# Optimization experiments

Hardware: AMD Instinct MI355X
Metric: run time of the kernel (lower is better)

## Reference

```python
import jax, jax.numpy as jnp
import numpy as np

N = 50000      # nodes
E = 800000     # edges (before self loops)
F_IN = 50      # PPI num_features
H = 4          # heads
C = 64         # hidden per head
NC = 121       # PPI num_classes
NEG_SLOPE = 0.2


def setup_inputs() -> dict:
    key = jax.random.key(0)
    ks = jax.random.split(key, 20)
    p = lambda k, shape: (jax.random.normal(k, shape, jnp.float32) * 0.1)
    x0 = jax.random.normal(ks[0], (N, F_IN), jnp.float32)
    edge_index = jax.random.randint(ks[1], (2, E), 0, N, dtype=jnp.int64)
    return dict(
        x0=x0, edge_index=edge_index,
        W1=p(ks[2], (F_IN, H * C)), as1=p(ks[3], (H, C)), ad1=p(ks[4], (H, C)),
        res1=p(ks[5], (F_IN, H * C)), b1=jnp.zeros((H * C,), jnp.float32),
        W2=p(ks[6], (H * C, H * C)), as2=p(ks[7], (H, C)), ad2=p(ks[8], (H, C)),
        res2=p(ks[9], (H * C, H * C)), b2=jnp.zeros((H * C,), jnp.float32),
        W3=p(ks[10], (H * C, H * NC)), as3=p(ks[11], (H, NC)), ad3=p(ks[12], (H, NC)),
        res3=p(ks[13], (H * C, NC)), b3=jnp.zeros((NC,), jnp.float32),
    )


def _gat(x, src, dst, W, a_src, a_dst, resW, b, concat):
    """PyG-style GATConv with residual, self loops already in (src, dst)."""
    n = x.shape[0]
    heads, outc = a_src.shape
    h = (x @ W).reshape(n, heads, outc)                 # [N,H,C]
    al_s = (h * a_src).sum(-1)                          # [N,H]
    al_d = (h * a_dst).sum(-1)                          # [N,H]
    e = jax.nn.leaky_relu(al_s[src] + al_d[dst], NEG_SLOPE)  # [E,H]
    m = jax.ops.segment_max(e, dst, num_segments=n)     # stable softmax per dst
    ex = jnp.exp(e - m[dst])
    denom = jax.ops.segment_sum(ex, dst, num_segments=n)
    alpha = ex / denom[dst]                             # [E,H]
    out = jax.ops.segment_sum(h[src] * alpha[:, :, None], dst, num_segments=n)  # [N,H,C]
    out = out.reshape(n, heads * outc) if concat else out.mean(axis=1)
    return out + x @ resW + b


def reference(x0, edge_index,
              W1, as1, ad1, res1, b1,
              W2, as2, ad2, res2, b2,
              W3, as3, ad3, res3, b3):
    n = x0.shape[0]
    loop = jnp.arange(n, dtype=edge_index.dtype)        # add self loops (PyG default)
    src = jnp.concatenate([edge_index[0], loop])
    dst = jnp.concatenate([edge_index[1], loop])
    x1 = jax.nn.relu(_gat(x0, src, dst, W1, as1, ad1, res1, b1, True))
    x2 = jax.nn.relu(_gat(x1, src, dst, W2, as2, ad2, res2, b2, True))
    x3 = _gat(x2, src, dst, W3, as3, ad3, res3, b3, False)
    return x3
```

## Files before the change

### kernel.cpp

```cpp
#include <hip/hip_runtime.h>

#define NNODES 50000
#define NEDGES 800000
#define NTOT   (NEDGES + NNODES)
#define F_IN   50
#define KPAD1  64
#define HEADS  4
#define C1     64
#define HC1    256
#define NC     121
#define K1S    320
#define K3S    1280
#define N2S    512

typedef unsigned short ushort_t;
typedef __attribute__((ext_vector_type(4))) unsigned short ushort4_t;
typedef __attribute__((ext_vector_type(8))) unsigned short ushort8;
typedef __attribute__((ext_vector_type(8))) __bf16 bf16x8;
typedef __attribute__((ext_vector_type(4))) float f32x4;
typedef __attribute__((ext_vector_type(4))) int int4_t;

__device__ __forceinline__ ushort_t f2bf(float f) {
    union { float f; unsigned int u; } v; v.f = f;
    unsigned int u = v.u;
// ... 139 lines not shown
        return;
    }
    i -= SZ_D;
    if (i < SZ_E) {
        int c = i / K3S, kk = i - c * K3S;
        float v;
        if (kk < 1024) {
            int h = kk >> 8, k = kk & 255;
            v = 0.25f * W3[(size_t)k * (HEADS * NC) + h * NC + c];
        } else {
            int k = kk - 1024;
            v = res3[(size_t)k * NC + c];
        }
        Bt3[i] = f2bf(v);
        return;
    }
    i -= SZ_E;
    if (i < 2 * SZ_F) {
        const float* a = (i < SZ_F) ? as1 : ad1;
        float* w = (i < SZ_F) ? w_as1 : w_ad1;
        int ii = (i < SZ_F) ? i : i - SZ_F;
        int k = ii >> 2, h = ii & 3;
        float s = 0.f;
        if (k < F_IN)
            for (int c = 0; c < C1; ++c) s += W1[(size_t)k * HC1 + h * C1 + c] * a[h * C1 + c];
        w[ii] = s;
        return;
    }
    i -= 2 * SZ_F;
    {
        int grp = i / SZ_G, ii = i - grp * SZ_G;
        int k = ii >> 2, h = ii & 3;
        float s = 0.f;
        if (grp < 2) {
            const float* a = grp ? ad2 : as2;
            for (int c = 0; c < C1; ++c) s += W2[(size_t)k * HC1 + h * C1 + c] * a[h * C1 + c];
            (grp ? w_ad2 : w_as2)[ii] = s;
        } else {
            const float* a = (grp == 3) ? ad3 : as3;
            for (int c = 0; c < NC; ++c) s += W3[(size_t)k * (HEADS * NC) + h * NC + c] * a[h * NC + c];
            ((grp == 3) ? w_ad3 : w_as3)[ii] = s;
        }
    }
}

__global__ __launch_bounds__(256)
void prep_count_kernel(const float* __restrict__ x0,
                 const float* __restrict__ W1, const float* __restrict__ res1,
                 const float* __restrict__ W2, const float* __restrict__ res2,
                 const float* __restrict__ W3, const float* __restrict__ res3,
                 const float* __restrict__ as1, const float* __restrict__ ad1,
                 const float* __restrict__ as2, const float* __restrict__ ad2,
                 const float* __restrict__ as3, const float* __restrict__ ad3,
                 const float* __restrict__ b2,
                 ushort_t* __restrict__ x0b, ushort_t* __restrict__ Bt1,
                 ushort_t* __restrict__ Bt2, ushort_t* __restrict__ Bt3,
                 float* __restrict__ bias512,
                 float* __restrict__ w_as1, float* __restrict__ w_ad1,
                 float* __restrict__ w_as2, float* __restrict__ w_ad2,
                 float* __restrict__ w_as3, float* __restrict__ w_ad3,
                 const int* __restrict__ ei, int* __restrict__ cnt) {
    int b = blockIdx.x;
    if (b < PREP_BLK) {
        prep_body(b * 256 + threadIdx.x, x0, W1, res1, W2, res2, W3, res3,
                  as1, ad1, as2, ad2, as3, ad3, b2, x0b, Bt1, Bt2, Bt3,
                  bias512, w_as1, w_ad1, w_as2, w_ad2, w_as3, w_ad3);
    } else {
        count_body((b - PREP_BLK) * 256 + threadIdx.x, ei, cnt);
    }
}

#define BM 128
#define BN 128
#define BK 64
#define LDP (BK + 8)

__global__ __launch_bounds__(256)
void gemm_mfma_kernel(const ushort_t* __restrict__ A1, int lda1,
                      const ushort_t* __restrict__ A2, int lda2, int Ksplit,
                      const ushort_t* __restrict__ Bt, const float* __restrict__ bias,
                      float* __restrict__ Cf, ushort_t* __restrict__ Cb,
                      int M, int N, int K, int relu) {
    __shared__ ushort_t As[BM * LDP];
    __shared__ ushort_t Bs[BN * LDP];
    int tid = threadIdx.x;
    int lane = tid & 63;
    int wid = tid >> 6;
    int wm = (wid & 1) * 64, wn = (wid >> 1) * 64;
    int l15 = lane & 15;
    int q8 = (lane >> 4) * 8;
    int m0 = blockIdx.y * BM, n0 = blockIdx.x * BN;

    f32x4 acc[4][4] = {};

    for (int k0 = 0; k0 < K; k0 += BK) {
        #pragma unroll
        for (int it = 0; it < 4; ++it) {
            int c = tid + it * 256;
            int row = c >> 3, c8 = c & 7;
            int k = k0 + c8 * 8;
            ushort8 va = (ushort8)0;
            int gm = m0 + row;
            if (gm < M) {
                if (k < Ksplit) va = *(const ushort8*)&A1[(size_t)gm * lda1 + k];
                else            va = *(const ushort8*)&A2[(size_t)gm * lda2 + (k - Ksplit)];
            }
            *(ushort8*)&As[row * LDP + c8 * 8] = va;
            ushort8 vb = (ushort8)0;
            int gn = n0 + row;
            if (gn < N) vb = *(const ushort8*)&Bt[(size_t)gn * K + k];
            *(ushort8*)&Bs[row * LDP + c8 * 8] = vb;
        }
        __syncthreads();
        #pragma unroll
        for (int kk = 0; kk < BK; kk += 32) {
            bf16x8 af[4], bfr[4];
            #pragma unroll
            for (int mi = 0; mi < 4; ++mi)
                af[mi] = *(const bf16x8*)&As[(wm + mi * 16 + l15) * LDP + kk + q8];
            #pragma unroll
            for (int ni = 0; ni < 4; ++ni)
                bfr[ni] = *(const bf16x8*)&Bs[(wn + ni * 16 + l15) * LDP + kk + q8];
            #pragma unroll
            for (int mi = 0; mi < 4; ++mi)
                #pragma unroll
                for (int ni = 0; ni < 4; ++ni)
                    acc[mi][ni] = __builtin_amdgcn_mfma_f32_16x16x32_bf16(
                        af[mi], bfr[ni], acc[mi][ni], 0, 0, 0);
        }
        __syncthreads();
    }

    #pragma unroll
    for (int mi = 0; mi < 4; ++mi) {
        int mbase = m0 + wm + mi * 16 + (lane >> 4) * 4;
        #pragma unroll
        for (int ni = 0; ni < 4; ++ni) {
            int ncol = n0 + wn + ni * 16 + l15;
            if (ncol >= N) continue;
            float bv = bias ? bias[ncol] : 0.f;
            #pragma unroll
            for (int r = 0; r < 4; ++r) {
                int m = mbase + r;
                if (m >= M) continue;
                float v = acc[mi][ni][r] + bv;
                if (relu) v = fmaxf(v, 0.f);
                if (Cf) Cf[(size_t)m * N + ncol] = v;
                else    Cb[(size_t)m * N + ncol] = f2bf(v);
            }
        }
    }
}

__device__ __forceinline__ void gemv_body(int n, int lane,
                        const ushort_t* __restrict__ X, int K,
                        const float* __restrict__ w_as, const float* __restrict__ w_ad,
                        float* __restrict__ als, float* __restrict__ ald) {
    float ps[HEADS] = {}, pd[HEADS] = {};
    for (int k0 = lane * 4; k0 < K; k0 += 256) {
        ushort4_t xv = *(const ushort4_t*)&X[(size_t)n * K + k0];
        float x[4] = {bf2f(xv.x), bf2f(xv.y), bf2f(xv.z), bf2f(xv.w)};
        #pragma unroll
        for (int j = 0; j < 4; ++j) {
            #pragma unroll
            for (int h = 0; h < HEADS; ++h) {
                ps[h] += x[j] * w_as[(k0 + j) * 4 + h];
                pd[h] += x[j] * w_ad[(k0 + j) * 4 + h];
            }
        }
    }
    #pragma unroll
    for (int off = 32; off; off >>= 1)
        #pragma unroll
        for (int h = 0; h < HEADS; ++h) {
            ps[h] += __shfl_xor(ps[h], off);
            pd[h] += __shfl_xor(pd[h], off);
        }
    if (lane == 0)
        #pragma unroll
        for (int h = 0; h < HEADS; ++h) {
            als[n * HEADS + h] = ps[h];
            ald[n * HEADS + h] = pd[h];
        }
}

__global__ __launch_bounds__(256)
void logits_gemv_kernel(const ushort_t* __restrict__ X, int K,
                        const float* __restrict__ w_as, const float* __restrict__ w_ad,
                        float* __restrict__ als, float* __restrict__ ald) {
    gemv_body(blockIdx.x * 4 + (threadIdx.x >> 6), threadIdx.x & 63, X, K, w_as, w_ad, als, ald);
}

#define GEMV_BLK (NNODES / 4)
__global__ __launch_bounds__(256)
void scatter_gemv1_kernel(const int* __restrict__ ei, int* __restrict__ cursor,
                          int* __restrict__ csr_src,
                          const ushort_t* __restrict__ X,
                          const float* __restrict__ w_as, const float* __restrict__ w_ad,
                          float* __restrict__ als, float* __restrict__ ald) {
    int b = blockIdx.x;
    if (b < GEMV_BLK) {
        gemv_body(b * 4 + (threadIdx.x >> 6), threadIdx.x & 63, X, KPAD1, w_as, w_ad, als, ald);
    } else {
        scatter_body((b - GEMV_BLK) * 256 + threadIdx.x, ei, cursor, csr_src);
    }
}

#define E_CHUNK_NOMAX(ROWBYTES)                                               \
    int i = base + lane;                                                      \
    int nv = end - base; if (nv > 64) nv = 64;                                \
    if (i < end) {                                                            \
        int s = csr_src[i];                                                   \
        soffw[lane] = s * (ROWBYTES);                                         \
        f32x4 av = *(const f32x4*)&als[s * 4];                                \
        f32x4 e;                                                              \
        _Pragma("unroll")                                                     \
        for (int h = 0; h < HEADS; ++h) {                                     \
            e[h] = __expf(lrelu(av[h] + aldd[h]));                            \
            den4[h] += e[h];                                                  \
        }                                                                     \
        *(f32x4*)&sew[lane * 4] = e;                                          \
    }                                                                         \
    wave_lds_sync();

#define DEN_REDUCE                                                            \
    _Pragma("unroll")                                                         \
    for (int off = 32; off; off >>= 1)                                        \
        _Pragma("unroll")                                                     \
        for (int h = 0; h < HEADS; ++h)                                       \
            den4[h] += __shfl_xor(den4[h], off);

#define AGG_BLOCKS 2048
#define AGG_WAVES  (AGG_BLOCKS * 4)

__global__ __launch_bounds__(256)
void agg1_kernel(const ushort_t* __restrict__ x0b,
                 const float* __restrict__ als, const float* __restrict__ ald,
                 const int* __restrict__ row_ptr, const int* __restrict__ csr_src,
                 ushort_t* __restrict__ aggx) {
    __shared__ int   soff[4][64];
    __shared__ float se[4][64 * 4];
    int wid = threadIdx.x >> 6, lane = threadIdx.x & 63;
    int* soffw = soff[wid];
    float* sew = se[wid];
    int lb = lane * 2;
    for (int d = blockIdx.x * 4 + wid; d < NNODES; d += AGG_WAVES) {
        int beg = row_ptr[d], end = row_ptr[d + 1];
        f32x4 aldd = *(const f32x4*)&ald[d * 4];
        f32x4 den4 = (f32x4)0.f;
        f32x4 acc  = (f32x4)0.f;
        for (int base = beg; base < end; base += 64) {
            E_CHUNK_NOMAX(KPAD1 * 2)
            int j = 0;
            for (; j + 4 <= nv; j += 4) {
                int4_t o = *(const int4_t*)&soffw[j];
                f32x4 e0 = *(const f32x4*)&sew[j * 4];
                f32x4 e1 = *(const f32x4*)&sew[(j + 1) * 4];
                f32x4 e2 = *(const f32x4*)&sew[(j + 2) * 4];
                f32x4 e3 = *(const f32x4*)&sew[(j + 3) * 4];
                float x0v = bf2f(*(const ushort_t*)((const char*)x0b + o.x + lb));
                float x1v = bf2f(*(const ushort_t*)((const char*)x0b + o.y + lb));
                float x2v = bf2f(*(const ushort_t*)((const char*)x0b + o.z + lb));
                float x3v = bf2f(*(const ushort_t*)((const char*)x0b + o.w + lb));
                acc += e0 * x0v + e1 * x1v + e2 * x2v + e3 * x3v;
            }
            for (; j < nv; ++j) {
                int o = soffw[j];
                f32x4 e = *(const f32x4*)&sew[j * 4];
                float xv = bf2f(*(const ushort_t*)((const char*)x0b + o + lb));
                acc += e * xv;
            }
            wave_lds_sync();
        }
        DEN_REDUCE
        #pragma unroll
        for (int h = 0; h < HEADS; ++h)
            aggx[(size_t)d * HC1 + h * 64 + lane] = f2bf(acc[h] / den4[h]);
    }
}

__global__ __launch_bounds__(256)
void agg2_kernel(const ushort_t* __restrict__ comb,
                 const float* __restrict__ als, const float* __restrict__ ald,
                 const int* __restrict__ row_ptr, const int* __restrict__ csr_src,
                 const float* __restrict__ w_as3, const float* __restrict__ w_ad3,
                 ushort_t* __restrict__ xnext,
                 float* __restrict__ als3, float* __restrict__ ald3) {
    __shared__ int   soff[4][64];
    __shared__ float se[4][64 * 4];
    int wid = threadIdx.x >> 6, lane = threadIdx.x & 63;
    int* soffw = soff[wid];
    float* sew = se[wid];
    int hh = lane >> 4;
    int lb = lane * 8;
    for (int d = blockIdx.x * 4 + wid; d < NNODES; d += AGG_WAVES) {
        int beg = row_ptr[d], end = row_ptr[d + 1];
        f32x4 aldd = *(const f32x4*)&ald[d * 4];
        f32x4 den4 = (f32x4)0.f;
        f32x4 acc  = (f32x4)0.f;
        for (int base = beg; base < end; base += 64) {
            E_CHUNK_NOMAX(N2S * 2)
            int j = 0;
            for (; j + 4 <= nv; j += 4) {
                int4_t o = *(const int4_t*)&soffw[j];
                float e0 = sew[j * 4 + hh], e1 = sew[(j + 1) * 4 + hh];
                float e2 = sew[(j + 2) * 4 + hh], e3 = sew[(j + 3) * 4 + hh];
                f32x4 x0v = cvt4(*(const ushort4_t*)((const char*)comb + o.x + lb));
                f32x4 x1v = cvt4(*(const ushort4_t*)((const char*)comb + o.y + lb));
                f32x4 x2v = cvt4(*(const ushort4_t*)((const char*)comb + o.z + lb));
                f32x4 x3v = cvt4(*(const ushort4_t*)((const char*)comb + o.w + lb));
                acc += e0 * x0v + e1 * x1v + e2 * x2v + e3 * x3v;
            }
            for (; j < nv; ++j) {
                int o = soffw[j];
                float e = sew[j * 4 + hh];
                acc += e * cvt4(*(const ushort4_t*)((const char*)comb + o + lb));
            }
            wave_lds_sync();
        }
        DEN_REDUCE
        float r = 1.f / den4[hh];
        ushort4_t rv = *(const ushort4_t*)&comb[(size_t)d * N2S + 256 + lane * 4];
        f32x4 resv = cvt4(rv);
        f32x4 vout;
        #pragma unroll
        for (int c = 0; c < 4; ++c) vout[c] = fmaxf(acc[c] * r + resv[c], 0.f);
        ushort4_t o4;
        o4.x = f2bf(vout[0]); o4.y = f2bf(vout[1]);
        o4.z = f2bf(vout[2]); o4.w = f2bf(vout[3]);
        *(ushort4_t*)&xnext[(size_t)d * HC1 + lane * 4] = o4;
        f32x4 ps = (f32x4)0.f, pd = (f32x4)0.f;
        #pragma unroll
        for (int j = 0; j < 4; ++j) {
            f32x4 wsj = *(const f32x4*)&w_as3[(lane * 4 + j) * 4];
            f32x4 wdj = *(const f32x4*)&w_ad3[(lane * 4 + j) * 4];
            ps += vout[j] * wsj;
            pd += vout[j] * wdj;
        }
        #pragma unroll
        for (int off = 32; off; off >>= 1) {
            #pragma unroll
            for (int h = 0; h < HEADS; ++h) {
                ps[h] += __shfl_xor(ps[h], off);
                pd[h] += __shfl_xor(pd[h], off);
            }
        }
        if (lane == 0) {
            *(f32x4*)&als3[d * 4] = ps;
            *(f32x4*)&ald3[d * 4] = pd;
        }
    }
}

__global__ __launch_bounds__(256)
void agg3_kernel(const ushort_t* __restrict__ x2b,
                 const float* __restrict__ als, const float* __restrict__ ald,
                 const int* __restrict__ row_ptr, const int* __restrict__ csr_src,
                 ushort_t* __restrict__ aggx) {
    __shared__ int   soff[4][64];
    __shared__ float se[4][64 * 4];
    int wid = threadIdx.x >> 6, lane = threadIdx.x & 63;
    int* soffw = soff[wid];
    float* sew = se[wid];
    int lb = lane * 8;
    for (int d = blockIdx.x * 4 + wid; d < NNODES; d += AGG_WAVES) {
        int beg = row_ptr[d], end = row_ptr[d + 1];
        f32x4 aldd = *(const f32x4*)&ald[d * 4];
        f32x4 den4 = (f32x4)0.f;
        f32x4 acc[HEADS] = {};
        for (int base = beg; base < end; base += 64) {
            E_CHUNK_NOMAX(HC1 * 2)
            int j = 0;
            for (; j + 4 <= nv; j += 4) {
                int4_t o = *(const int4_t*)&soffw[j];
                f32x4 e0 = *(const f32x4*)&sew[j * 4];
                f32x4 e1 = *(const f32x4*)&sew[(j + 1) * 4];
                f32x4 e2 = *(const f32x4*)&sew[(j + 2) * 4];
                f32x4 e3 = *(const f32x4*)&sew[(j + 3) * 4];
                f32x4 x0v = cvt4(*(const ushort4_t*)((const char*)x2b + o.x + lb));
                f32x4 x1v = cvt4(*(const ushort4_t*)((const char*)x2b + o.y + lb));
                f32x4 x2v = cvt4(*(const ushort4_t*)((const char*)x2b + o.z + lb));
                f32x4 x3v = cvt4(*(const ushort4_t*)((const char*)x2b + o.w + lb));
                #pragma unroll
                for (int h = 0; h < HEADS; ++h)
                    acc[h] += e0[h] * x0v + e1[h] * x1v + e2[h] * x2v + e3[h] * x3v;
            }
            for (; j < nv; ++j) {
                int o = soffw[j];
                f32x4 e = *(const f32x4*)&sew[j * 4];
                f32x4 xv = cvt4(*(const ushort4_t*)((const char*)x2b + o + lb));
                #pragma unroll
                for (int h = 0; h < HEADS; ++h) acc[h] += e[h] * xv;
            }
            wave_lds_sync();
        }
        DEN_REDUCE
        #pragma unroll
        for (int h = 0; h < HEADS; ++h) {
            float rdv = 1.f / den4[h];
            ushort4_t o4;
            o4.x = f2bf(acc[h][0] * rdv); o4.y = f2bf(acc[h][1] * rdv);
            o4.z = f2bf(acc[h][2] * rdv); o4.w = f2bf(acc[h][3] * rdv);
            *(ushort4_t*)&aggx[(size_t)d * 1024 + h * HC1 + lane * 4] = o4;
        }
    }
}

extern "C" void kernel_launch(void* const* d_in, const int* in_sizes, int n_in,
                              void* d_out, int out_size, void* d_ws, size_t ws_size,
                              hipStream_t stream) {
    const float* x0   = (const float*)d_in[0];
    const int*   ei   = (const int*)d_in[1];
    const float* W1   = (const float*)d_in[2];
    const float* as1  = (const float*)d_in[3];
    const float* ad1  = (const float*)d_in[4];
    const float* res1 = (const float*)d_in[5];
    const float* b1   = (const float*)d_in[6];
    const float* W2   = (const float*)d_in[7];
    const float* as2  = (const float*)d_in[8];
    const float* ad2  = (const float*)d_in[9];
    const float* res2 = (const float*)d_in[10];
    const float* b2   = (const float*)d_in[11];
    const float* W3   = (const float*)d_in[12];
    const float* as3  = (const float*)d_in[13];
    const float* ad3  = (const float*)d_in[14];
    const float* res3 = (const float*)d_in[15];
    const float* b3   = (const float*)d_in[16];

    char* p = (char*)d_ws;
    auto alloc = [&](size_t bytes) -> void* {
        void* r = (void*)p;
        p += (bytes + 255) & ~(size_t)255;
        return r;
    };
    int*      cnt     = (int*)alloc((size_t)NNODES * 4);
    int*      incl    = (int*)alloc((size_t)NNODES * 4);
    int*      bsums   = (int*)alloc((size_t)SCB * 4);
    int*      row_ptr = (int*)alloc((size_t)(NNODES + 1) * 4);
    int*      cursor  = (int*)alloc((size_t)NNODES * 4);
    int*      csr_src = (int*)alloc((size_t)NTOT * 4);
    float*    als     = (float*)alloc((size_t)NNODES * HEADS * 4);
    float*    ald     = (float*)alloc((size_t)NNODES * HEADS * 4);
    float*    als3    = (float*)alloc((size_t)NNODES * HEADS * 4);
    float*    ald3    = (float*)alloc((size_t)NNODES * HEADS * 4);
    ushort_t* x0b     = (ushort_t*)alloc((size_t)NNODES * KPAD1 * 2);
    ushort_t* x2      = (ushort_t*)alloc((size_t)NNODES * HC1 * 2);
    ushort_t* Bt1     = (ushort_t*)alloc((size_t)HC1 * K1S * 2);
    ushort_t* Bt2     = (ushort_t*)alloc((size_t)N2S * HC1 * 2);
    float*    bias512 = (float*)alloc((size_t)N2S * 4);
    ushort_t* Bt3     = (ushort_t*)alloc((size_t)NC * K3S * 2);
    float*    w_as1   = (float*)alloc((size_t)KPAD1 * 4 * 4);
    float*    w_ad1   = (float*)alloc((size_t)KPAD1 * 4 * 4);
    float*    w_as2   = (float*)alloc((size_t)HC1 * 4 * 4);
    float*    w_ad2   = (float*)alloc((size_t)HC1 * 4 * 4);
    float*    w_as3   = (float*)alloc((size_t)HC1 * 4 * 4);
    float*    w_ad3   = (float*)alloc((size_t)HC1 * 4 * 4);
    char*     big     = (char*)alloc((size_t)NNODES * 1024 * 2);
    ushort_t* aggx1   = (ushort_t*)big;
    ushort_t* x1      = (ushort_t*)(big + (size_t)NNODES * HC1 * 2);
    ushort_t* comb    = (ushort_t*)(big + (size_t)NNODES * HC1 * 4);
    ushort_t* aggx3   = (ushort_t*)big;

    hipMemsetAsync(cnt, 0, (size_t)NNODES * 4, stream);

    int nscan = (NNODES + SCB - 1) / SCB;

    prep_count_kernel<<<PREP_BLK + CNT_BLK, 256, 0, stream>>>(
        x0, W1, res1, W2, res2, W3, res3, as1, ad1, as2, ad2, as3, ad3, b2,
        x0b, Bt1, Bt2, Bt3, bias512, w_as1, w_ad1, w_as2, w_ad2, w_as3, w_ad3,
        ei, cnt);
    scan1_kernel<<<nscan, SCB, 0, stream>>>(cnt, incl, bsums, NNODES);
    scan2_kernel<<<1, SCB, 0, stream>>>(bsums, nscan);
    scan3_kernel<<<nscan, SCB, 0, stream>>>(cnt, incl, bsums, row_ptr, cursor, NNODES);
    scatter_gemv1_kernel<<<GEMV_BLK + CNT_BLK, 256, 0, stream>>>(
        ei, cursor, csr_src, x0b, w_as1, w_ad1, als, ald);

    auto gemm = [&](const ushort_t* A1, int lda1, const ushort_t* A2, int lda2, int Ksplit,
                    const ushort_t* Bt, const float* bias,
                    float* Cf, ushort_t* Cb, int M, int Nn, int K, int relu) {
        dim3 g((Nn + BN - 1) / BN, (M + BM - 1) / BM);
        gemm_mfma_kernel<<<g, 256, 0, stream>>>(A1, lda1, A2, lda2, Ksplit, Bt, bias,
                                                Cf, Cb, M, Nn, K, relu);
    };

    int nagg = NNODES / 4;

    agg1_kernel<<<AGG_BLOCKS, 256, 0, stream>>>(x0b, als, ald, row_ptr, csr_src, aggx1);
    gemm(aggx1, HC1, x0b, KPAD1, HC1, Bt1, b1, nullptr, x1, NNODES, HC1, K1S, 1);

    gemm(x1, HC1, x1, HC1, HC1, Bt2, bias512, nullptr, comb, NNODES, N2S, HC1, 0);
    logits_gemv_kernel<<<nagg, 256, 0, stream>>>(x1, HC1, w_as2, w_ad2, als, ald);
    agg2_kernel<<<AGG_BLOCKS, 256, 0, stream>>>(comb, als, ald, row_ptr, csr_src,
                                                w_as3, w_ad3, x2, als3, ald3);

    agg3_kernel<<<AGG_BLOCKS, 256, 0, stream>>>(x2, als3, ald3, row_ptr, csr_src, aggx3);
    gemm(aggx3, 1024, x2, HC1, 1024, Bt3, b3, (float*)d_out, nullptr, NNODES, NC, K3S, 0);
}
```

Baseline: 659.9 us.

## Fuse layer-1 and layer-3 aggregation with their projection GEMMs via LDS tiles

The layer-1 and layer-3 aggregation kernels now each gather 16 destination rows into a shared-memory A tile, together with the residual input columns. Each block then runs the MFMA projection against Bt1/Bt3 directly, writing x1 (bias+ReLU) or the final output. This drops the separate GEMM launches and the global round trip of the aggx intermediates, which are large for layer 3 (1024 bf16 columns per node). Agg2 switches from a grid-stride loop to one node per wave. The costs are heavy LDS use in agg3mm (about 41KB) that limits occupancy, B-operand loads straight from global with no LDS reuse, and a poorly utilised layer-3 MFMA when 121 columns are spread across four waves.

Measured after the change: 686.2 us. 1.04x slower.

```diff
diff --git a/kernel.cpp b/kernel.cpp
--- a/kernel.cpp
+++ b/kernel.cpp
@@ -393,21 +393,24 @@
         for (int h = 0; h < HEADS; ++h)                                       \
             den4[h] += __shfl_xor(den4[h], off);
 
-#define AGG_BLOCKS 2048
-#define AGG_WAVES  (AGG_BLOCKS * 4)
-
+#define LDP1 328
 __global__ __launch_bounds__(256)
-void agg1_kernel(const ushort_t* __restrict__ x0b,
-                 const float* __restrict__ als, const float* __restrict__ ald,
-                 const int* __restrict__ row_ptr, const int* __restrict__ csr_src,
-                 ushort_t* __restrict__ aggx) {
+void agg1mm_kernel(const ushort_t* __restrict__ x0b,
+                   const float* __restrict__ als, const float* __restrict__ ald,
+                   const int* __restrict__ row_ptr, const int* __restrict__ csr_src,
+                   const ushort_t* __restrict__ Bt1, const float* __restrict__ b1,
+                   ushort_t* __restrict__ x1out) {
+    __shared__ ushort_t A[16][LDP1];
     __shared__ int   soff[4][64];
     __shared__ float se[4][64 * 4];
     int wid = threadIdx.x >> 6, lane = threadIdx.x & 63;
     int* soffw = soff[wid];
     float* sew = se[wid];
+    int d0 = blockIdx.x * 16;
     int lb = lane * 2;
-    for (int d = blockIdx.x * 4 + wid; d < NNODES; d += AGG_WAVES) {
+    for (int nn = 0; nn < 4; ++nn) {
+        int row = wid * 4 + nn;
+        int d = d0 + row;
         int beg = row_ptr[d], end = row_ptr[d + 1];
         f32x4 aldd = *(const f32x4*)&ald[d * 4];
         f32x4 den4 = (f32x4)0.f;
@@ -438,7 +441,30 @@
         DEN_REDUCE
         #pragma unroll
         for (int h = 0; h < HEADS; ++h)
-            aggx[(size_t)d * HC1 + h * 64 + lane] = f2bf(acc[h] / den4[h]);
+            A[row][h * 64 + lane] = f2bf(acc[h] / den4[h]);
+        A[row][256 + lane] = x0b[(size_t)d * KPAD1 + lane];
+    }
+    __syncthreads();
+    int l15 = lane & 15, q8 = (lane >> 4) * 8, wn = wid * 64;
+    f32x4 c4[4] = {};
+    for (int kk = 0; kk < K1S; kk += 32) {
+        bf16x8 af = *(const bf16x8*)&A[l15][kk + q8];
+        #pragma unroll
+        for (int ni = 0; ni < 4; ++ni) {
+            bf16x8 bf = *(const bf16x8*)&Bt1[(size_t)(wn + ni * 16 + l15) * K1S + kk + q8];
+            c4[ni] = __builtin_amdgcn_mfma_f32_16x16x32_bf16(af, bf, c4[ni], 0, 0, 0);
+        }
+    }
+    int rbase = (lane >> 4) * 4;
+    #pragma unroll
+    for (int ni = 0; ni < 4; ++ni) {
+        int col = wn + ni * 16 + l15;
+        float bv = b1[col];
+        #pragma unroll
+        for (int r = 0; r < 4; ++r) {
+            float v = fmaxf(c4[ni][r] + bv, 0.f);
+            x1out[(size_t)(d0 + rbase + r) * HC1 + col] = f2bf(v);
+        }
     }
 }
 
@@ -452,81 +478,86 @@
     __shared__ int   soff[4][64];
     __shared__ float se[4][64 * 4];
     int wid = threadIdx.x >> 6, lane = threadIdx.x & 63;
+    int d = blockIdx.x * 4 + wid;
     int* soffw = soff[wid];
     float* sew = se[wid];
     int hh = lane >> 4;
+    int beg = row_ptr[d], end = row_ptr[d + 1];
+    f32x4 aldd = *(const f32x4*)&ald[d * 4];
+    f32x4 den4 = (f32x4)0.f;
+    f32x4 acc  = (f32x4)0.f;
     int lb = lane * 8;
-    for (int d = blockIdx.x * 4 + wid; d < NNODES; d += AGG_WAVES) {
-        int beg = row_ptr[d], end = row_ptr[d + 1];
-        f32x4 aldd = *(const f32x4*)&ald[d * 4];
-        f32x4 den4 = (f32x4)0.f;
-        f32x4 acc  = (f32x4)0.f;
-        for (int base = beg; base < end; base += 64) {
-            E_CHUNK_NOMAX(N2S * 2)
-            int j = 0;
-            for (; j + 4 <= nv; j += 4) {
-                int4_t o = *(const int4_t*)&soffw[j];
-                float e0 = sew[j * 4 + hh], e1 = sew[(j + 1) * 4 + hh];
-                float e2 = sew[(j + 2) * 4 + hh], e3 = sew[(j + 3) * 4 + hh];
-                f32x4 x0v = cvt4(*(const ushort4_t*)((const char*)comb + o.x + lb));
-                f32x4 x1v = cvt4(*(const ushort4_t*)((const char*)comb + o.y + lb));
-                f32x4 x2v = cvt4(*(const ushort4_t*)((const char*)comb + o.z + lb));
-                f32x4 x3v = cvt4(*(const ushort4_t*)((const char*)comb + o.w + lb));
-                acc += e0 * x0v + e1 * x1v + e2 * x2v + e3 * x3v;
-            }
-            for (; j < nv; ++j) {
-                int o = soffw[j];
-                float e = sew[j * 4 + hh];
-                acc += e * cvt4(*(const ushort4_t*)((const char*)comb + o + lb));
-            }
-            wave_lds_sync();
-        }
-        DEN_REDUCE
-        float r = 1.f / den4[hh];
-        ushort4_t rv = *(const ushort4_t*)&comb[(size_t)d * N2S + 256 + lane * 4];
-        f32x4 resv = cvt4(rv);
-        f32x4 vout;
-        #pragma unroll
-        for (int c = 0; c < 4; ++c) vout[c] = fmaxf(acc[c] * r + resv[c], 0.f);
-        ushort4_t o4;
-        o4.x = f2bf(vout[0]); o4.y = f2bf(vout[1]);
-        o4.z = f2bf(vout[2]); o4.w = f2bf(vout[3]);
-        *(ushort4_t*)&xnext[(size_t)d * HC1 + lane * 4] = o4;
-        f32x4 ps = (f32x4)0.f, pd = (f32x4)0.f;
-        #pragma unroll
-        for (int j = 0; j < 4; ++j) {
-            f32x4 wsj = *(const f32x4*)&w_as3[(lane * 4 + j) * 4];
-            f32x4 wdj = *(const f32x4*)&w_ad3[(lane * 4 + j) * 4];
-            ps += vout[j] * wsj;
-            pd += vout[j] * wdj;
-        }
-        #pragma unroll
-        for (int off = 32; off; off >>= 1) {
-            #pragma unroll
-            for (int h = 0; h < HEADS; ++h) {
-                ps[h] += __shfl_xor(ps[h], off);
-                pd[h] += __shfl_xor(pd[h], off);
-            }
-        }
-        if (lane == 0) {
-            *(f32x4*)&als3[d * 4] = ps;
-            *(f32x4*)&ald3[d * 4] = pd;
-        }
-    }
-}
-
+    for (int base = beg; base < end; base += 64) {
+        E_CHUNK_NOMAX(N2S * 2)
+        int j = 0;
+        for (; j + 4 <= nv; j += 4) {
+            int4_t o = *(const int4_t*)&soffw[j];
+            float e0 = sew[j * 4 + hh], e1 = sew[(j + 1) * 4 + hh];
+            float e2 = sew[(j + 2) * 4 + hh], e3 = sew[(j + 3) * 4 + hh];
+            f32x4 x0v = cvt4(*(const ushort4_t*)((const char*)comb + o.x + lb));
+            f32x4 x1v = cvt4(*(const ushort4_t*)((const char*)comb + o.y + lb));
+            f32x4 x2v = cvt4(*(const ushort4_t*)((const char*)comb + o.z + lb));
+            f32x4 x3v = cvt4(*(const ushort4_t*)((const char*)comb + o.w + lb));
+            acc += e0 * x0v + e1 * x1v + e2 * x2v + e3 * x3v;
+        }
+        for (; j < nv; ++j) {
+            int o = soffw[j];
+            float e = sew[j * 4 + hh];
+            acc += e * cvt4(*(const ushort4_t*)((const char*)comb + o + lb));
+        }
+        wave_lds_sync();
+    }
+    DEN_REDUCE
+    float r = 1.f / den4[hh];
+    ushort4_t rv = *(const ushort4_t*)&comb[(size_t)d * N2S + 256 + lane * 4];
+    f32x4 resv = cvt4(rv);
+    f32x4 vout;
+    #pragma unroll
+    for (int c = 0; c < 4; ++c) vout[c] = fmaxf(acc[c] * r + resv[c], 0.f);
+    ushort4_t o4;
+    o4.x = f2bf(vout[0]); o4.y = f2bf(vout[1]);
+    o4.z = f2bf(vout[2]); o4.w = f2bf(vout[3]);
+    *(ushort4_t*)&xnext[(size_t)d * HC1 + lane * 4] = o4;
+    f32x4 ps = (f32x4)0.f, pd = (f32x4)0.f;
+    #pragma unroll
+    for (int j = 0; j < 4; ++j) {
+        f32x4 wsj = *(const f32x4*)&w_as3[(lane * 4 + j) * 4];
+        f32x4 wdj = *(const f32x4*)&w_ad3[(lane * 4 + j) * 4];
+        ps += vout[j] * wsj;
+        pd += vout[j] * wdj;
+    }
+    #pragma unroll
+    for (int off = 32; off; off >>= 1) {
+        #pragma unroll
+        for (int h = 0; h < HEADS; ++h) {
+            ps[h] += __shfl_xor(ps[h], off);
+            pd[h] += __shfl_xor(pd[h], off);
+        }
+    }
+    if (lane == 0) {
+        *(f32x4*)&als3[d * 4] = ps;
+        *(f32x4*)&ald3[d * 4] = pd;
+    }
+}
+
+#define LDP3 1288
 __global__ __launch_bounds__(256)
-void agg3_kernel(const ushort_t* __restrict__ x2b,
-                 const float* __restrict__ als, const float* __restrict__ ald,
-                 const int* __restrict__ row_ptr, const int* __restrict__ csr_src,
-                 ushort_t* __restrict__ aggx) {
+void agg3mm_kernel(const ushort_t* __restrict__ x2b,
+                   const float* __restrict__ als, const float* __restrict__ ald,
+                   const int* __restrict__ row_ptr, const int* __restrict__ csr_src,
+                   const ushort_t* __restrict__ Bt3, const float* __restrict__ b3,
+                   float* __restrict__ out) {
+    __shared__ ushort_t A[16][LDP3];
     __shared__ int   soff[4][64];
     __shared__ float se[4][64 * 4];
     int wid = threadIdx.x >> 6, lane = threadIdx.x & 63;
     int* soffw = soff[wid];
     float* sew = se[wid];
+    int d0 = blockIdx.x * 16;
     int lb = lane * 8;
-    for (int d = blockIdx.x * 4 + wid; d < NNODES; d += AGG_WAVES) {
+    for (int nn = 0; nn < 4; ++nn) {
+        int row = wid * 4 + nn;
+        int d = d0 + row;
         int beg = row_ptr[d], end = row_ptr[d + 1];
         f32x4 aldd = *(const f32x4*)&ald[d * 4];
         f32x4 den4 = (f32x4)0.f;
@@ -564,8 +595,31 @@
             ushort4_t o4;
             o4.x = f2bf(acc[h][0] * rdv); o4.y = f2bf(acc[h][1] * rdv);
             o4.z = f2bf(acc[h][2] * rdv); o4.w = f2bf(acc[h][3] * rdv);
-            *(ushort4_t*)&aggx[(size_t)d * 1024 + h * HC1 + lane * 4] = o4;
-        }
+            *(ushort4_t*)&A[row][h * 256 + lane * 4] = o4;
+        }
+        *(ushort4_t*)&A[row][1024 + lane * 4] =
+            *(const ushort4_t*)&x2b[(size_t)d * HC1 + lane * 4];
+    }
+    __syncthreads();
+    int l15 = lane & 15, q8 = (lane >> 4) * 8, wn = wid * 32;
+    f32x4 c4[2] = {};
+    for (int kk = 0; kk < K3S; kk += 32) {
+        bf16x8 af = *(const bf16x8*)&A[l15][kk + q8];
+        #pragma unroll
+        for (int ni = 0; ni < 2; ++ni) {
+            bf16x8 bf = *(const bf16x8*)&Bt3[(size_t)(wn + ni * 16 + l15) * K3S + kk + q8];
+            c4[ni] = __builtin_amdgcn_mfma_f32_16x16x32_bf16(af, bf, c4[ni], 0, 0, 0);
+        }
+    }
+    int rbase = (lane >> 4) * 4;
+    #pragma unroll
+    for (int ni = 0; ni < 2; ++ni) {
+        int col = wn + ni * 16 + l15;
+        if (col >= NC) continue;
+        float bv = b3[col];
+        #pragma unroll
+        for (int r = 0; r < 4; ++r)
+            out[(size_t)(d0 + rbase + r) * NC + col] = c4[ni][r] + bv;
     }
 }
 
@@ -618,11 +672,8 @@
     float*    w_ad2   = (float*)alloc((size_t)HC1 * 4 * 4);
     float*    w_as3   = (float*)alloc((size_t)HC1 * 4 * 4);
     float*    w_ad3   = (float*)alloc((size_t)HC1 * 4 * 4);
-    char*     big     = (char*)alloc((size_t)NNODES * 1024 * 2);
-    ushort_t* aggx1   = (ushort_t*)big;
-    ushort_t* x1      = (ushort_t*)(big + (size_t)NNODES * HC1 * 2);
-    ushort_t* comb    = (ushort_t*)(big + (size_t)NNODES * HC1 * 4);
-    ushort_t* aggx3   = (ushort_t*)big;
+    ushort_t* x1      = (ushort_t*)alloc((size_t)NNODES * HC1 * 2);
+    ushort_t* comb    = (ushort_t*)alloc((size_t)NNODES * N2S * 2);
 
     hipMemsetAsync(cnt, 0, (size_t)NNODES * 4, stream);
 
@@ -638,24 +689,21 @@
     scatter_gemv1_kernel<<<GEMV_BLK + CNT_BLK, 256, 0, stream>>>(
         ei, cursor, csr_src, x0b, w_as1, w_ad1, als, ald);
 
-    auto gemm = [&](const ushort_t* A1, int lda1, const ushort_t* A2, int lda2, int Ksplit,
-                    const ushort_t* Bt, const float* bias,
-                    float* Cf, ushort_t* Cb, int M, int Nn, int K, int relu) {
-        dim3 g((Nn + BN - 1) / BN, (M + BM - 1) / BM);
-        gemm_mfma_kernel<<<g, 256, 0, stream>>>(A1, lda1, A2, lda2, Ksplit, Bt, bias,
-                                                Cf, Cb, M, Nn, K, relu);
-    };
-
     int nagg = NNODES / 4;
-
-    agg1_kernel<<<AGG_BLOCKS, 256, 0, stream>>>(x0b, als, ald, row_ptr, csr_src, aggx1);
-    gemm(aggx1, HC1, x0b, KPAD1, HC1, Bt1, b1, nullptr, x1, NNODES, HC1, K1S, 1);
-
-    gemm(x1, HC1, x1, HC1, HC1, Bt2, bias512, nullptr, comb, NNODES, N2S, HC1, 0);
+    int nfus = NNODES / 16;
+
+    agg1mm_kernel<<<nfus, 256, 0, stream>>>(x0b, als, ald, row_ptr, csr_src,
+                                            Bt1, b1, x1);
+
+    {
+        dim3 g((N2S + BN - 1) / BN, (NNODES + BM - 1) / BM);
+        gemm_mfma_kernel<<<g, 256, 0, stream>>>(x1, HC1, x1, HC1, HC1, Bt2, bias512,
+                                                nullptr, comb, NNODES, N2S, HC1, 0);
+    }
     logits_gemv_kernel<<<nagg, 256, 0, stream>>>(x1, HC1, w_as2, w_ad2, als, ald);
-    agg2_kernel<<<AGG_BLOCKS, 256, 0, stream>>>(comb, als, ald, row_ptr, csr_src,
-                                                w_as3, w_ad3, x2, als3, ald3);
-
-    agg3_kernel<<<AGG_BLOCKS, 256, 0, stream>>>(x2, als3, ald3, row_ptr, csr_src, aggx3);
-    gemm(aggx3, 1024, x2, HC1, 1024, Bt3, b3, (float*)d_out, nullptr, NNODES, NC, K3S, 0);
-}
+    agg2_kernel<<<nagg, 256, 0, stream>>>(comb, als, ald, row_ptr, csr_src,
+                                          w_as3, w_ad3, x2, als3, ald3);
+
+    agg3mm_kernel<<<nfus, 256, 0, stream>>>(x2, als3, ald3, row_ptr, csr_src,
+                                            Bt3, b3, (float*)d_out);
+}
```

## Software-pipeline aggregation gathers, one node per wave, specialized final GEMM

Applied to the files above, without the earlier changes.

The three aggregation kernels now give each wave exactly one destination node instead of a grid-stride loop. Their inner loops are software-pipelined so the next group of four neighbour gathers is issued before the current group is accumulated. The last layer's projection moves to a dedicated MFMA kernel whose 64-row tile covers all 121 output columns in one block, replacing the generic tiled GEMM. Both aim to hide gather latency and cut GEMM tile overhead, at the cost of more registers for the prefetched values and a much larger launch grid.

Result: faster. 629.8 us (-4.6%).

```diff
diff --git a/kernel.cpp b/kernel.cpp
--- a/kernel.cpp
+++ b/kernel.cpp
@@ -315,6 +315,66 @@
     }
 }
 
+__global__ __launch_bounds__(256)
+void gemm3s_kernel(const ushort_t* __restrict__ A1, int lda1,
+                   const ushort_t* __restrict__ A2, int lda2, int Ksplit,
+                   const ushort_t* __restrict__ Bt, const float* __restrict__ bias,
+                   float* __restrict__ out, int M, int N, int K) {
+    __shared__ ushort_t As[64 * LDP];
+    __shared__ ushort_t Bs[128 * LDP];
+    int tid = threadIdx.x, lane = tid & 63, wid = tid >> 6;
+    int l15 = lane & 15, q8 = (lane >> 4) * 8;
+    int m0 = blockIdx.x * 64;
+    f32x4 c4[8] = {};
+    for (int k0 = 0; k0 < K; k0 += BK) {
+        #pragma unroll
+        for (int it = 0; it < 2; ++it) {
+            int c = tid + it * 256;
+            int row = c >> 3, c8 = c & 7;
+            int k = k0 + c8 * 8;
+            ushort8 va = (ushort8)0;
+            int gm = m0 + row;
+            if (gm < M) {
+                if (k < Ksplit) va = *(const ushort8*)&A1[(size_t)gm * lda1 + k];
+                else            va = *(const ushort8*)&A2[(size_t)gm * lda2 + (k - Ksplit)];
+            }
+            *(ushort8*)&As[row * LDP + c8 * 8] = va;
+        }
+        #pragma unroll
+        for (int it = 0; it < 4; ++it) {
+            int c = tid + it * 256;
+            int row = c >> 3, c8 = c & 7;
+            int k = k0 + c8 * 8;
+            ushort8 vb = (ushort8)0;
+            if (row < N) vb = *(const ushort8*)&Bt[(size_t)row * K + k];
+            *(ushort8*)&Bs[row * LDP + c8 * 8] = vb;
+        }
+        __syncthreads();
+        #pragma unroll
+        for (int kk = 0; kk < BK; kk += 32) {
+            bf16x8 af = *(const bf16x8*)&As[(wid * 16 + l15) * LDP + kk + q8];
+            #pragma unroll
+            for (int ni = 0; ni < 8; ++ni) {
+                bf16x8 bf = *(const bf16x8*)&Bs[(ni * 16 + l15) * LDP + kk + q8];
+                c4[ni] = __builtin_amdgcn_mfma_f32_16x16x32_bf16(af, bf, c4[ni], 0, 0, 0);
+            }
+        }
+        __syncthreads();
+    }
+    int rbase = m0 + wid * 16 + (lane >> 4) * 4;
+    #pragma unroll
+    for (int ni = 0; ni < 8; ++ni) {
+        int col = ni * 16 + l15;
+        if (col >= NC) continue;
+        float bv = bias[col];
+        #pragma unroll
+        for (int r = 0; r < 4; ++r) {
+            int m = rbase + r;
+            if (m < M) out[(size_t)m * NC + col] = c4[ni][r] + bv;
+        }
+    }
+}
+
 __device__ __forceinline__ void gemv_body(int n, int lane,
                         const ushort_t* __restrict__ X, int K,
                         const float* __restrict__ w_as, const float* __restrict__ w_ad,
@@ -393,9 +453,6 @@
         for (int h = 0; h < HEADS; ++h)                                       \
             den4[h] += __shfl_xor(den4[h], off);
 
-#define AGG_BLOCKS 2048
-#define AGG_WAVES  (AGG_BLOCKS * 4)
-
 __global__ __launch_bounds__(256)
 void agg1_kernel(const ushort_t* __restrict__ x0b,
                  const float* __restrict__ als, const float* __restrict__ ald,
@@ -404,42 +461,56 @@
     __shared__ int   soff[4][64];
     __shared__ float se[4][64 * 4];
     int wid = threadIdx.x >> 6, lane = threadIdx.x & 63;
+    int d = blockIdx.x * 4 + wid;
     int* soffw = soff[wid];
     float* sew = se[wid];
+    int beg = row_ptr[d], end = row_ptr[d + 1];
+    f32x4 aldd = *(const f32x4*)&ald[d * 4];
+    f32x4 den4 = (f32x4)0.f;
+    f32x4 acc  = (f32x4)0.f;
     int lb = lane * 2;
-    for (int d = blockIdx.x * 4 + wid; d < NNODES; d += AGG_WAVES) {
-        int beg = row_ptr[d], end = row_ptr[d + 1];
-        f32x4 aldd = *(const f32x4*)&ald[d * 4];
-        f32x4 den4 = (f32x4)0.f;
-        f32x4 acc  = (f32x4)0.f;
-        for (int base = beg; base < end; base += 64) {
-            E_CHUNK_NOMAX(KPAD1 * 2)
-            int j = 0;
-            for (; j + 4 <= nv; j += 4) {
-                int4_t o = *(const int4_t*)&soffw[j];
-                f32x4 e0 = *(const f32x4*)&sew[j * 4];
-                f32x4 e1 = *(const f32x4*)&sew[(j + 1) * 4];
-                f32x4 e2 = *(const f32x4*)&sew[(j + 2) * 4];
-                f32x4 e3 = *(const f32x4*)&sew[(j + 3) * 4];
-                float x0v = bf2f(*(const ushort_t*)((const char*)x0b + o.x + lb));
-                float x1v = bf2f(*(const ushort_t*)((const char*)x0b + o.y + lb));
-                float x2v = bf2f(*(const ushort_t*)((const char*)x0b + o.z + lb));
-                float x3v = bf2f(*(const ushort_t*)((const char*)x0b + o.w + lb));
-                acc += e0 * x0v + e1 * x1v + e2 * x2v + e3 * x3v;
+    for (int base = beg; base < end; base += 64) {
+        E_CHUNK_NOMAX(KPAD1 * 2)
+        int j = 0;
+        if (nv >= 4) {
+            int4_t o = *(const int4_t*)&soffw[0];
+            ushort_t v0 = *(const ushort_t*)((const char*)x0b + o.x + lb);
+            ushort_t v1 = *(const ushort_t*)((const char*)x0b + o.y + lb);
+            ushort_t v2 = *(const ushort_t*)((const char*)x0b + o.z + lb);
+            ushort_t v3 = *(const ushort_t*)((const char*)x0b + o.w + lb);
+            for (j = 4; j + 4 <= nv; j += 4) {
+                int4_t on = *(const int4_t*)&soffw[j];
+                ushort_t w0 = *(const ushort_t*)((const char*)x0b + on.x + lb);
+                ushort_t w1 = *(const ushort_t*)((const char*)x0b + on.y + lb);
+                ushort_t w2 = *(const ushort_t*)((const char*)x0b + on.z + lb);
+                ushort_t w3 = *(const ushort_t*)((const char*)x0b + on.w + lb);
+                int jj = j - 4;
+                f32x4 e0 = *(const f32x4*)&sew[jj * 4];
+                f32x4 e1 = *(const f32x4*)&sew[(jj + 1) * 4];
+                f32x4 e2 = *(const f32x4*)&sew[(jj + 2) * 4];
+                f32x4 e3 = *(const f32x4*)&sew[(jj + 3) * 4];
+                acc += e0 * bf2f(v0) + e1 * bf2f(v1) + e2 * bf2f(v2) + e3 * bf2f(v3);
+                v0 = w0; v1 = w1; v2 = w2; v3 = w3;
             }
-            for (; j < nv; ++j) {
-                int o = soffw[j];
-                f32x4 e = *(const f32x4*)&sew[j * 4];
-                float xv = bf2f(*(const ushort_t*)((const char*)x0b + o + lb));
-                acc += e * xv;
-            }
-            wave_lds_sync();
-        }
-        DEN_REDUCE
-        #pragma unroll
-        for (int h = 0; h < HEADS; ++h)
-            aggx[(size_t)d * HC1 + h * 64 + lane] = f2bf(acc[h] / den4[h]);
-    }
+            int jj = j - 4;
+            f32x4 e0 = *(const f32x4*)&sew[jj * 4];
+            f32x4 e1 = *(const f32x4*)&sew[(jj + 1) * 4];
+            f32x4 e2 = *(const f32x4*)&sew[(jj + 2) * 4];
+            f32x4 e3 = *(const f32x4*)&sew[(jj + 3) * 4];
+            acc += e0 * bf2f(v0) + e1 * bf2f(v1) + e2 * bf2f(v2) + e3 * bf2f(v3);
+        }
+        for (; j < nv; ++j) {
+            int o = soffw[j];
+            f32x4 e = *(const f32x4*)&sew[j * 4];
+            float xv = bf2f(*(const ushort_t*)((const char*)x0b + o + lb));
+            acc += e * xv;
+        }
+        wave_lds_sync();
+    }
+    DEN_REDUCE
+    #pragma unroll
+    for (int h = 0; h < HEADS; ++h)
+        aggx[(size_t)d * HC1 + h * 64 + lane] = f2bf(acc[h] / den4[h]);
 }
 
 __global__ __launch_bounds__(256)
@@ -452,66 +523,78 @@
     __shared__ int   soff[4][64];
     __shared__ float se[4][64 * 4];
     int wid = threadIdx.x >> 6, lane = threadIdx.x & 63;
+    int d = blockIdx.x * 4 + wid;
     int* soffw = soff[wid];
     float* sew = se[wid];
     int hh = lane >> 4;
+    int beg = row_ptr[d], end = row_ptr[d + 1];
+    f32x4 aldd = *(const f32x4*)&ald[d * 4];
+    f32x4 den4 = (f32x4)0.f;
+    f32x4 acc  = (f32x4)0.f;
     int lb = lane * 8;
-    for (int d = blockIdx.x * 4 + wid; d < NNODES; d += AGG_WAVES) {
-        int beg = row_ptr[d], end = row_ptr[d + 1];
-        f32x4 aldd = *(const f32x4*)&ald[d * 4];
-        f32x4 den4 = (f32x4)0.f;
-        f32x4 acc  = (f32x4)0.f;
-        for (int base = beg; base < end; base += 64) {
-            E_CHUNK_NOMAX(N2S * 2)
-            int j = 0;
-            for (; j + 4 <= nv; j += 4) {
-                int4_t o = *(const int4_t*)&soffw[j];
-                float e0 = sew[j * 4 + hh], e1 = sew[(j + 1) * 4 + hh];
-                float e2 = sew[(j + 2) * 4 + hh], e3 = sew[(j + 3) * 4 + hh];
-                f32x4 x0v = cvt4(*(const ushort4_t*)((const char*)comb + o.x + lb));
-                f32x4 x1v = cvt4(*(const ushort4_t*)((const char*)comb + o.y + lb));
-                f32x4 x2v = cvt4(*(const ushort4_t*)((const char*)comb + o.z + lb));
-                f32x4 x3v = cvt4(*(const ushort4_t*)((const char*)comb + o.w + lb));
-                acc += e0 * x0v + e1 * x1v + e2 * x2v + e3 * x3v;
+    for (int base = beg; base < end; base += 64) {
+        E_CHUNK_NOMAX(N2S * 2)
+        int j = 0;
+        if (nv >= 4) {
+            int4_t o = *(const int4_t*)&soffw[0];
+            ushort4_t v0 = *(const ushort4_t*)((const char*)comb + o.x + lb);
+            ushort4_t v1 = *(const ushort4_t*)((const char*)comb + o.y + lb);
+            ushort4_t v2 = *(const ushort4_t*)((const char*)comb + o.z + lb);
+            ushort4_t v3 = *(const ushort4_t*)((const char*)comb + o.w + lb);
+            for (j = 4; j + 4 <= nv; j += 4) {
+                int4_t on = *(const int4_t*)&soffw[j];
+                ushort4_t w0 = *(const ushort4_t*)((const char*)comb + on.x + lb);
+                ushort4_t w1 = *(const ushort4_t*)((const char*)comb + on.y + lb);
+                ushort4_t w2 = *(const ushort4_t*)((const char*)comb + on.z + lb);
+                ushort4_t w3 = *(const ushort4_t*)((const char*)comb + on.w + lb);
+                int jj = j - 4;
+                float e0 = sew[jj * 4 + hh], e1 = sew[(jj + 1) * 4 + hh];
+                float e2 = sew[(jj + 2) * 4 + hh], e3 = sew[(jj + 3) * 4 + hh];
+                acc += e0 * cvt4(v0) + e1 * cvt4(v1) + e2 * cvt4(v2) + e3 * cvt4(v3);
+                v0 = w0; v1 = w1; v2 = w2; v3 = w3;
             }
-            for (; j < nv; ++j) {
-                int o = soffw[j];
-                float e = sew[j * 4 + hh];
-                acc += e * cvt4(*(const ushort4_t*)((const char*)comb + o + lb));
-            }
-            wave_lds_sync();
-        }
-        DEN_REDUCE
-        float r = 1.f / den4[hh];
-        ushort4_t rv = *(const ushort4_t*)&comb[(size_t)d * N2S + 256 + lane * 4];
-        f32x4 resv = cvt4(rv);
-        f32x4 vout;
-        #pragma unroll
-        for (int c = 0; c < 4; ++c) vout[c] = fmaxf(acc[c] * r + resv[c], 0.f);
-        ushort4_t o4;
-        o4.x = f2bf(vout[0]); o4.y = f2bf(vout[1]);
-        o4.z = f2bf(vout[2]); o4.w = f2bf(vout[3]);
-        *(ushort4_t*)&xnext[(size_t)d * HC1 + lane * 4] = o4;
-        f32x4 ps = (f32x4)0.f, pd = (f32x4)0.f;
-        #pragma unroll
-        for (int j = 0; j < 4; ++j) {
-            f32x4 wsj = *(const f32x4*)&w_as3[(lane * 4 + j) * 4];
-            f32x4 wdj = *(const f32x4*)&w_ad3[(lane * 4 + j) * 4];
-            ps += vout[j] * wsj;
-            pd += vout[j] * wdj;
-        }
-        #pragma unroll
-        for (int off = 32; off; off >>= 1) {
-            #pragma unroll
-            for (int h = 0; h < HEADS; ++h) {
-                ps[h] += __shfl_xor(ps[h], off);
-                pd[h] += __shfl_xor(pd[h], off);
-            }
-        }
-        if (lane == 0) {
-            *(f32x4*)&als3[d * 4] = ps;
-            *(f32x4*)&ald3[d * 4] = pd;
-        }
+            int jj = j - 4;
+            float e0 = sew[jj * 4 + hh], e1 = sew[(jj + 1) * 4 + hh];
+            float e2 = sew[(jj + 2) * 4 + hh], e3 = sew[(jj + 3) * 4 + hh];
+            acc += e0 * cvt4(v0) + e1 * cvt4(v1) + e2 * cvt4(v2) + e3 * cvt4(v3);
+        }
+        for (; j < nv; ++j) {
+            int o = soffw[j];
+            float e = sew[j * 4 + hh];
+            acc += e * cvt4(*(const ushort4_t*)((const char*)comb + o + lb));
+        }
+        wave_lds_sync();
+    }
+    DEN_REDUCE
+    float r = 1.f / den4[hh];
+    ushort4_t rv = *(const ushort4_t*)&comb[(size_t)d * N2S + 256 + lane * 4];
+    f32x4 resv = cvt4(rv);
+    f32x4 vout;
+    #pragma unroll
+    for (int c = 0; c < 4; ++c) vout[c] = fmaxf(acc[c] * r + resv[c], 0.f);
+    ushort4_t o4;
+    o4.x = f2bf(vout[0]); o4.y = f2bf(vout[1]);
+    o4.z = f2bf(vout[2]); o4.w = f2bf(vout[3]);
+    *(ushort4_t*)&xnext[(size_t)d * HC1 + lane * 4] = o4;
+    f32x4 ps = (f32x4)0.f, pd = (f32x4)0.f;
+    #pragma unroll
+    for (int j = 0; j < 4; ++j) {
+        f32x4 wsj = *(const f32x4*)&w_as3[(lane * 4 + j) * 4];
+        f32x4 wdj = *(const f32x4*)&w_ad3[(lane * 4 + j) * 4];
+        ps += vout[j] * wsj;
+        pd += vout[j] * wdj;
+    }
+    #pragma unroll
+    for (int off = 32; off; off >>= 1) {
+        #pragma unroll
+        for (int h = 0; h < HEADS; ++h) {
+            ps[h] += __shfl_xor(ps[h], off);
+            pd[h] += __shfl_xor(pd[h], off);
+        }
+    }
+    if (lane == 0) {
+        *(f32x4*)&als3[d * 4] = ps;
+        *(f32x4*)&ald3[d * 4] = pd;
     }
 }
 
@@ -523,49 +606,67 @@
     __shared__ int   soff[4][64];
     __shared__ float se[4][64 * 4];
     int wid = threadIdx.x >> 6, lane = threadIdx.x & 63;
+    int d = blockIdx.x * 4 + wid;
     int* soffw = soff[wid];
     float* sew = se[wid];
+    int beg = row_ptr[d], end = row_ptr[d + 1];
+    f32x4 aldd = *(const f32x4*)&ald[d * 4];
+    f32x4 den4 = (f32x4)0.f;
+    f32x4 acc[HEADS] = {};
     int lb = lane * 8;
-    for (int d = blockIdx.x * 4 + wid; d < NNODES; d += AGG_WAVES) {
-        int beg = row_ptr[d], end = row_ptr[d + 1];
-        f32x4 aldd = *(const f32x4*)&ald[d * 4];
-        f32x4 den4 = (f32x4)0.f;
-        f32x4 acc[HEADS] = {};
-        for (int base = beg; base < end; base += 64) {
-            E_CHUNK_NOMAX(HC1 * 2)
-            int j = 0;
-            for (; j + 4 <= nv; j += 4) {
-                int4_t o = *(const int4_t*)&soffw[j];
-                f32x4 e0 = *(const f32x4*)&sew[j * 4];
-                f32x4 e1 = *(const f32x4*)&sew[(j + 1) * 4];
-                f32x4 e2 = *(const f32x4*)&sew[(j + 2) * 4];
-                f32x4 e3 = *(const f32x4*)&sew[(j + 3) * 4];
-                f32x4 x0v = cvt4(*(const ushort4_t*)((const char*)x2b + o.x + lb));
-                f32x4 x1v = cvt4(*(const ushort4_t*)((const char*)x2b + o.y + lb));
-                f32x4 x2v = cvt4(*(const ushort4_t*)((const char*)x2b + o.z + lb));
-                f32x4 x3v = cvt4(*(const ushort4_t*)((const char*)x2b + o.w + lb));
+    for (int base = beg; base < end; base += 64) {
+        E_CHUNK_NOMAX(HC1 * 2)
+        int j = 0;
+        if (nv >= 4) {
+            int4_t o = *(const int4_t*)&soffw[0];
+            ushort4_t v0 = *(const ushort4_t*)((const char*)x2b + o.x + lb);
+            ushort4_t v1 = *(const ushort4_t*)((const char*)x2b + o.y + lb);
+            ushort4_t v2 = *(const ushort4_t*)((const char*)x2b + o.z + lb);
+            ushort4_t v3 = *(const ushort4_t*)((const char*)x2b + o.w + lb);
+            for (j = 4; j + 4 <= nv; j += 4) {
+                int4_t on = *(const int4_t*)&soffw[j];
+                ushort4_t w0 = *(const ushort4_t*)((const char*)x2b + on.x + lb);
+                ushort4_t w1 = *(const ushort4_t*)((const char*)x2b + on.y + lb);
+                ushort4_t w2 = *(const ushort4_t*)((const char*)x2b + on.z + lb);
+                ushort4_t w3 = *(const ushort4_t*)((const char*)x2b + on.w + lb);
+                int jj = j - 4;
+                f32x4 e0 = *(const f32x4*)&sew[jj * 4];
+                f32x4 e1 = *(const f32x4*)&sew[(jj + 1) * 4];
+                f32x4 e2 = *(const f32x4*)&sew[(jj + 2) * 4];
+                f32x4 e3 = *(const f32x4*)&sew[(jj + 3) * 4];
+                f32x4 x0v = cvt4(v0), x1v = cvt4(v1), x2v = cvt4(v2), x3v = cvt4(v3);
                 #pragma unroll
                 for (int h = 0; h < HEADS; ++h)
                     acc[h] += e0[h] * x0v + e1[h] * x1v + e2[h] * x2v + e3[h] * x3v;
+                v0 = w0; v1 = w1; v2 = w2; v3 = w3;
             }
-            for (; j < nv; ++j) {
-                int o = soffw[j];
-                f32x4 e = *(const f32x4*)&sew[j * 4];
-                f32x4 xv = cvt4(*(const ushort4_t*)((const char*)x2b + o + lb));
-                #pragma unroll
-                for (int h = 0; h < HEADS; ++h) acc[h] += e[h] * xv;
-            }
-            wave_lds_sync();
-        }
-        DEN_REDUCE
-        #pragma unroll
-        for (int h = 0; h < HEADS; ++h) {
-            float rdv = 1.f / den4[h];
-            ushort4_t o4;
-            o4.x = f2bf(acc[h][0] * rdv); o4.y = f2bf(acc[h][1] * rdv);
-            o4.z = f2bf(acc[h][2] * rdv); o4.w = f2bf(acc[h][3] * rdv);
-            *(ushort4_t*)&aggx[(size_t)d * 1024 + h * HC1 + lane * 4] = o4;
-        }
+            int jj = j - 4;
+            f32x4 e0 = *(const f32x4*)&sew[jj * 4];
+            f32x4 e1 = *(const f32x4*)&sew[(jj + 1) * 4];
+            f32x4 e2 = *(const f32x4*)&sew[(jj + 2) * 4];
+            f32x4 e3 = *(const f32x4*)&sew[(jj + 3) * 4];
+            f32x4 x0v = cvt4(v0), x1v = cvt4(v1), x2v = cvt4(v2), x3v = cvt4(v3);
+            #pragma unroll
+            for (int h = 0; h < HEADS; ++h)
+                acc[h] += e0[h] * x0v + e1[h] * x1v + e2[h] * x2v + e3[h] * x3v;
+        }
+        for (; j < nv; ++j) {
+            int o = soffw[j];
+            f32x4 e = *(const f32x4*)&sew[j * 4];
+            f32x4 xv = cvt4(*(const ushort4_t*)((const char*)x2b + o + lb));
+            #pragma unroll
+            for (int h = 0; h < HEADS; ++h) acc[h] += e[h] * xv;
+        }
+        wave_lds_sync();
+    }
+    DEN_REDUCE
+    #pragma unroll
+    for (int h = 0; h < HEADS; ++h) {
+        float rdv = 1.f / den4[h];
+        ushort4_t o4;
+        o4.x = f2bf(acc[h][0] * rdv); o4.y = f2bf(acc[h][1] * rdv);
+        o4.z = f2bf(acc[h][2] * rdv); o4.w = f2bf(acc[h][3] * rdv);
+        *(ushort4_t*)&aggx[(size_t)d * 1024 + h * HC1 + lane * 4] = o4;
     }
 }
 
@@ -648,14 +749,15 @@
 
     int nagg = NNODES / 4;
 
-    agg1_kernel<<<AGG_BLOCKS, 256, 0, stream>>>(x0b, als, ald, row_ptr, csr_src, aggx1);
+    agg1_kernel<<<nagg, 256, 0, stream>>>(x0b, als, ald, row_ptr, csr_src, aggx1);
     gemm(aggx1, HC1, x0b, KPAD1, HC1, Bt1, b1, nullptr, x1, NNODES, HC1, K1S, 1);
 
     gemm(x1, HC1, x1, HC1, HC1, Bt2, bias512, nullptr, comb, NNODES, N2S, HC1, 0);
     logits_gemv_kernel<<<nagg, 256, 0, stream>>>(x1, HC1, w_as2, w_ad2, als, ald);
-    agg2_kernel<<<AGG_BLOCKS, 256, 0, stream>>>(comb, als, ald, row_ptr, csr_src,
-                                                w_as3, w_ad3, x2, als3, ald3);
-
-    agg3_kernel<<<AGG_BLOCKS, 256, 0, stream>>>(x2, als3, ald3, row_ptr, csr_src, aggx3);
-    gemm(aggx3, 1024, x2, HC1, 1024, Bt3, b3, (float*)d_out, nullptr, NNODES, NC, K3S, 0);
-}
+    agg2_kernel<<<nagg, 256, 0, stream>>>(comb, als, ald, row_ptr, csr_src,
+                                          w_as3, w_ad3, x2, als3, ald3);
+
+    agg3_kernel<<<nagg, 256, 0, stream>>>(x2, als3, ald3, row_ptr, csr_src, aggx3);
+    gemm3s_kernel<<<(NNODES + 63) / 64, 256, 0, stream>>>(
+        aggx3, 1024, x2, HC1, 1024, Bt3, b3, (float*)d_out, NNODES, 128, K3S);
+}
```
